# Kernel optimization log

Measured on AMD Instinct MI355X. Metric: run time of the kernel, lower is better.

The kernel has to match this reference:

```python
import jax, jax.numpy as jnp
import numpy as np

N = 100000      # nodes
DEG = 16        # in-degree per node
E = N * DEG     # edges
IN_DIM = 128
OUT_DIM = 32
EPS = 1e-8      # torch cosine_similarity norm clamp


def setup_inputs() -> dict:
    key = jax.random.key(0)
    k1, k2, k3, k4 = jax.random.split(key, 4)
    h = jax.random.normal(k1, (N, IN_DIM), dtype=jnp.float32)
    # xavier_uniform-scaled linear weight, shape [out_dim, in_dim] like nn.Linear
    W = jax.random.normal(k2, (OUT_DIM, IN_DIM), dtype=jnp.float32) * (1.0 / np.sqrt(IN_DIM))
    beta = jax.random.uniform(k3, (1,), dtype=jnp.float32)
    src = jax.random.randint(k4, (E,), 0, N)
    dst = jnp.arange(E) // DEG  # each node gets exactly DEG incoming edges
    return {"h": h, "W": W, "beta": beta, "src": src, "dst": dst}


def reference(h, W, beta, src, dst):
    # Note: F.dropout(p=0.6) from the original is omitted for a deterministic reference.
    z = h @ W.T                                   # [N, out_dim]
    zs = z[src]                                   # [E, out_dim] gather src features
    zd = z[dst]                                   # [E, out_dim] gather dst features
    num = jnp.sum(zs * zd, axis=-1)               # [E]
    ns = jnp.maximum(jnp.linalg.norm(zs, axis=-1), EPS)
    nd = jnp.maximum(jnp.linalg.norm(zd, axis=-1), EPS)
    cos = num / (ns * nd)                         # torch.cosine_similarity
    e = -beta[0] * (1.0 - cos)                    # [E] edge score
    # segment softmax over incoming edges of each dst node (stable)
    m = jax.ops.segment_max(e, dst, num_segments=N)
    m = jnp.where(jnp.isfinite(m), m, 0.0)        # guard isolated nodes
    ex = jnp.exp(e - m[dst])                      # [E]
    denom = jax.ops.segment_sum(ex, dst, num_segments=N)
    alpha = ex / denom[dst]                       # [E] attention weights
    # weighted scatter-sum of src features to dst nodes
    return jax.ops.segment_sum(alpha[:, None] * zs, dst, num_segments=N)  # [N, out_dim]
```

## Files before the change

### kernel.cpp

```cpp
#include <hip/hip_runtime.h>

#define IN_DIM 128
#define OUT_DIM 32
#define DEG 16
#define EPS 1e-8f
#define TN 64
#define HSTR 129

#define SWZ(x, p) __int_as_float(__builtin_amdgcn_ds_swizzle(__float_as_int(x), (p)))

__global__ __launch_bounds__(256) void gemm_norm_kernel(
    const float* __restrict__ h, const float* __restrict__ W,
    float* __restrict__ z, float* __restrict__ inv_nrm, int N) {
  __shared__ float sh[TN * HSTR];
  __shared__ float ssq[4][TN];

  const int tid = threadIdx.x;
  const int nb = blockIdx.x * TN;

  const float4* __restrict__ hg = (const float4*)h;
#pragma unroll
  for (int i = 0; i < 8; ++i) {
    const int f = tid + 256 * i;
    const int nd = f >> 5;
    const int k4 = f & 31;
    int gn = nb + nd;
    if (gn >= N) gn = N - 1;
    const float4 v = hg[(size_t)gn * 32 + k4];
    float* d = &sh[nd * HSTR + k4 * 4];
    d[0] = v.x; d[1] = v.y; d[2] = v.z; d[3] = v.w;
  }
  __syncthreads();

  const int w = __builtin_amdgcn_readfirstlane(tid >> 6);
  const int l = tid & 63;
  const int node = nb + l;
  const float* __restrict__ wb = W + (size_t)(w * 8) * IN_DIM;
  const float* hrow = &sh[l * HSTR];

  float acc[8] = {0.f, 0.f, 0.f, 0.f, 0.f, 0.f, 0.f, 0.f};
#pragma unroll 8
  for (int k = 0; k < IN_DIM; ++k) {
    const float hv = hrow[k];
#pragma unroll
    for (int j = 0; j < 8; ++j)
      acc[j] = fmaf(hv, wb[j * IN_DIM + k], acc[j]);
  }

  float ssp = 0.f;
#pragma unroll
  for (int j = 0; j < 8; ++j) ssp = fmaf(acc[j], acc[j], ssp);
  ssq[w][l] = ssp;

  if (node < N) {
    float4* zp = (float4*)(z + (size_t)node * OUT_DIM + w * 8);
    zp[0] = make_float4(acc[0], acc[1], acc[2], acc[3]);
    zp[1] = make_float4(acc[4], acc[5], acc[6], acc[7]);
  }
  __syncthreads();
  if (w == 0) {
    const float s = ssq[0][l] + ssq[1][l] + ssq[2][l] + ssq[3][l];
    if (node < N) inv_nrm[node] = 1.0f / fmaxf(sqrtf(s), EPS);
  }
}

__global__ __launch_bounds__(256) void edge_kernel(
    const float* __restrict__ z, const float* __restrict__ inv_nrm,
    const int* __restrict__ src, const float* __restrict__ beta_p,
    float* __restrict__ out, int N) {
  __shared__ float xp[4 * 2 * DEG * 36];

  const int tid = threadIdx.x;
  const int l = tid & 63, l5 = l & 31, half = l >> 5, wv = tid >> 6;
  const int gw = blockIdx.x * 4 + wv;
  if (gw * 2 >= N) return;
  const int n = gw * 2 + half;
  const int ne = (n < N) ? n : N - 1;
  const int e = l5 >> 1, c = l5 & 1;

  const float beta = *beta_p;
  const int se = src[(size_t)ne * DEG + e];
  const float inv_s = inv_nrm[se];
  const float inv_d = inv_nrm[ne];

  const float4* zs4 = (const float4*)(z + (size_t)se * OUT_DIM + c * 16);
  const float4 v0 = zs4[0], v1 = zs4[1], v2 = zs4[2], v3 = zs4[3];
  const float4* zd4 = (const float4*)(z + (size_t)ne * OUT_DIM + c * 16);
  const float4 d0 = zd4[0], d1 = zd4[1], d2 = zd4[2], d3 = zd4[3];

  float p = v0.x * d0.x;
  p = fmaf(v0.y, d0.y, p); p = fmaf(v0.z, d0.z, p); p = fmaf(v0.w, d0.w, p);
  p = fmaf(v1.x, d1.x, p); p = fmaf(v1.y, d1.y, p); p = fmaf(v1.z, d1.z, p);
  p = fmaf(v1.w, d1.w, p);
  p = fmaf(v2.x, d2.x, p); p = fmaf(v2.y, d2.y, p); p = fmaf(v2.z, d2.z, p);
  p = fmaf(v2.w, d2.w, p);
  p = fmaf(v3.x, d3.x, p); p = fmaf(v3.y, d3.y, p); p = fmaf(v3.z, d3.z, p);
  p = fmaf(v3.w, d3.w, p);
  p += SWZ(p, 0x041F);

  const float cosv = p * inv_s * inv_d;
  const float ex = __expf(beta * (cosv - 1.0f));

  float den = ex;
  den += SWZ(den, 0x081F);
  den += SWZ(den, 0x101F);
  den += SWZ(den, 0x201F);
  den += SWZ(den, 0x401F);
  const float rd = 1.0f / den;

  float* slot = xp + (wv * 2 + half) * (DEG * 36);
  float4* wp = (float4*)(slot + e * 36 + c * 16);
  wp[0] = make_float4(ex * v0.x, ex * v0.y, ex * v0.z, ex * v0.w);
  wp[1] = make_float4(ex * v1.x, ex * v1.y, ex * v1.z, ex * v1.w);
  wp[2] = make_float4(ex * v2.x, ex * v2.y, ex * v2.z, ex * v2.w);
  wp[3] = make_float4(ex * v3.x, ex * v3.y, ex * v3.z, ex * v3.w);

  float s = 0.f;
#pragma unroll
  for (int e2 = 0; e2 < DEG; ++e2)
    s += slot[e2 * 36 + l5];

  if (n < N) out[(size_t)n * OUT_DIM + l5] = s * rd;
}

extern "C" void kernel_launch(void* const* d_in, const int* in_sizes, int n_in,
                              void* d_out, int out_size, void* d_ws, size_t ws_size,
                              hipStream_t stream) {
  const float* h    = (const float*)d_in[0];
  const float* W    = (const float*)d_in[1];
  const float* beta = (const float*)d_in[2];
  const int*   src  = (const int*)d_in[3];

  const int N = in_sizes[0] / IN_DIM;

  float* z    = (float*)d_ws;
  float* invn = z + (size_t)N * OUT_DIM;

  const int bl1 = (N + TN - 1) / TN;
  gemm_norm_kernel<<<bl1, 256, 0, stream>>>(h, W, z, invn, N);

  const int waves2 = (N + 1) / 2;
  const int bl2 = (waves2 + 3) / 4;
  edge_kernel<<<bl2, 256, 0, stream>>>(z, invn, src, beta, (float*)d_out, N);
}
```

Measured before the change: 139.1 us.

## Store pre-normalized z as bf16 and transpose h tile for float4 LDS reads

```diff
diff --git a/kernel.cpp b/kernel.cpp
--- a/kernel.cpp
+++ b/kernel.cpp
@@ -5,73 +5,87 @@
 #define DEG 16
 #define EPS 1e-8f
 #define TN 64
-#define HSTR 129
+#define S4 65
 
 #define SWZ(x, p) __int_as_float(__builtin_amdgcn_ds_swizzle(__float_as_int(x), (p)))
 
+static __device__ __forceinline__ unsigned f2bf(float x) {
+  unsigned u = __float_as_uint(x);
+  u += 0x7FFFu + ((u >> 16) & 1u);
+  return u >> 16;
+}
+static __device__ __forceinline__ float bflo(unsigned u) { return __uint_as_float(u << 16); }
+static __device__ __forceinline__ float bfhi(unsigned u) { return __uint_as_float(u & 0xFFFF0000u); }
+
 __global__ __launch_bounds__(256) void gemm_norm_kernel(
     const float* __restrict__ h, const float* __restrict__ W,
-    float* __restrict__ z, float* __restrict__ inv_nrm, int N) {
-  __shared__ float sh[TN * HSTR];
+    unsigned short* __restrict__ zhb, float* __restrict__ nrm, int N) {
+  __shared__ float4 sh4[32 * S4];
   __shared__ float ssq[4][TN];
 
   const int tid = threadIdx.x;
   const int nb = blockIdx.x * TN;
 
-  const float4* __restrict__ hg = (const float4*)h;
+  {
+    const int k4 = tid & 31, r0 = tid >> 5;
+    const float4* __restrict__ hg = (const float4*)h;
 #pragma unroll
-  for (int i = 0; i < 8; ++i) {
-    const int f = tid + 256 * i;
-    const int nd = f >> 5;
-    const int k4 = f & 31;
-    int gn = nb + nd;
-    if (gn >= N) gn = N - 1;
-    const float4 v = hg[(size_t)gn * 32 + k4];
-    float* d = &sh[nd * HSTR + k4 * 4];
-    d[0] = v.x; d[1] = v.y; d[2] = v.z; d[3] = v.w;
+    for (int i = 0; i < 8; ++i) {
+      const int n = r0 + i * 8;
+      int gn = nb + n;
+      if (gn >= N) gn = N - 1;
+      sh4[k4 * S4 + n] = hg[(size_t)gn * 32 + k4];
+    }
   }
   __syncthreads();
 
-  const int w = __builtin_amdgcn_readfirstlane(tid >> 6);
+  const int w = tid >> 6;
   const int l = tid & 63;
   const int node = nb + l;
   const float* __restrict__ wb = W + (size_t)(w * 8) * IN_DIM;
-  const float* hrow = &sh[l * HSTR];
 
   float acc[8] = {0.f, 0.f, 0.f, 0.f, 0.f, 0.f, 0.f, 0.f};
-#pragma unroll 8
-  for (int k = 0; k < IN_DIM; ++k) {
-    const float hv = hrow[k];
+#pragma unroll 4
+  for (int k4 = 0; k4 < 32; ++k4) {
+    const float4 hv = sh4[k4 * S4 + l];
 #pragma unroll
-    for (int j = 0; j < 8; ++j)
-      acc[j] = fmaf(hv, wb[j * IN_DIM + k], acc[j]);
+    for (int j = 0; j < 8; ++j) {
+      const float* __restrict__ wr = wb + j * IN_DIM + k4 * 4;
+      acc[j] = fmaf(hv.x, wr[0], acc[j]);
+      acc[j] = fmaf(hv.y, wr[1], acc[j]);
+      acc[j] = fmaf(hv.z, wr[2], acc[j]);
+      acc[j] = fmaf(hv.w, wr[3], acc[j]);
+    }
   }
 
   float ssp = 0.f;
 #pragma unroll
   for (int j = 0; j < 8; ++j) ssp = fmaf(acc[j], acc[j], ssp);
   ssq[w][l] = ssp;
+  __syncthreads();
+  const float ss = ssq[0][l] + ssq[1][l] + ssq[2][l] + ssq[3][l];
+  const float ns = sqrtf(ss);
+  const float inv = 1.0f / fmaxf(ns, EPS);
 
   if (node < N) {
-    float4* zp = (float4*)(z + (size_t)node * OUT_DIM + w * 8);
-    zp[0] = make_float4(acc[0], acc[1], acc[2], acc[3]);
-    zp[1] = make_float4(acc[4], acc[5], acc[6], acc[7]);
-  }
-  __syncthreads();
-  if (w == 0) {
-    const float s = ssq[0][l] + ssq[1][l] + ssq[2][l] + ssq[3][l];
-    if (node < N) inv_nrm[node] = 1.0f / fmaxf(sqrtf(s), EPS);
+    unsigned p0 = f2bf(acc[0] * inv) | (f2bf(acc[1] * inv) << 16);
+    unsigned p1 = f2bf(acc[2] * inv) | (f2bf(acc[3] * inv) << 16);
+    unsigned p2 = f2bf(acc[4] * inv) | (f2bf(acc[5] * inv) << 16);
+    unsigned p3 = f2bf(acc[6] * inv) | (f2bf(acc[7] * inv) << 16);
+    uint4* zp = (uint4*)(zhb + (size_t)node * OUT_DIM + w * 8);
+    *zp = make_uint4(p0, p1, p2, p3);
+    if (w == 0) nrm[node] = ns;
   }
 }
 
 __global__ __launch_bounds__(256) void edge_kernel(
-    const float* __restrict__ z, const float* __restrict__ inv_nrm,
+    const unsigned short* __restrict__ zhb, const float* __restrict__ nrm,
     const int* __restrict__ src, const float* __restrict__ beta_p,
     float* __restrict__ out, int N) {
-  __shared__ float xp[4 * 2 * DEG * 36];
+  __shared__ float xp[8 * DEG * 36];
 
   const int tid = threadIdx.x;
-  const int l = tid & 63, l5 = l & 31, half = l >> 5, wv = tid >> 6;
+  const int l5 = tid & 31, half = (tid >> 5) & 1, wv = tid >> 6;
   const int gw = blockIdx.x * 4 + wv;
   if (gw * 2 >= N) return;
   const int n = gw * 2 + half;
@@ -80,26 +94,30 @@
 
   const float beta = *beta_p;
   const int se = src[(size_t)ne * DEG + e];
-  const float inv_s = inv_nrm[se];
-  const float inv_d = inv_nrm[ne];
+  const float nrm_s = nrm[se];
 
-  const float4* zs4 = (const float4*)(z + (size_t)se * OUT_DIM + c * 16);
-  const float4 v0 = zs4[0], v1 = zs4[1], v2 = zs4[2], v3 = zs4[3];
-  const float4* zd4 = (const float4*)(z + (size_t)ne * OUT_DIM + c * 16);
-  const float4 d0 = zd4[0], d1 = zd4[1], d2 = zd4[2], d3 = zd4[3];
+  const uint4* zs4 = (const uint4*)(zhb + (size_t)se * OUT_DIM) + c * 2;
+  const uint4 sa = zs4[0], sb = zs4[1];
+  const uint4* zd4 = (const uint4*)(zhb + (size_t)ne * OUT_DIM) + c * 2;
+  const uint4 da = zd4[0], db = zd4[1];
 
-  float p = v0.x * d0.x;
-  p = fmaf(v0.y, d0.y, p); p = fmaf(v0.z, d0.z, p); p = fmaf(v0.w, d0.w, p);
-  p = fmaf(v1.x, d1.x, p); p = fmaf(v1.y, d1.y, p); p = fmaf(v1.z, d1.z, p);
-  p = fmaf(v1.w, d1.w, p);
-  p = fmaf(v2.x, d2.x, p); p = fmaf(v2.y, d2.y, p); p = fmaf(v2.z, d2.z, p);
-  p = fmaf(v2.w, d2.w, p);
-  p = fmaf(v3.x, d3.x, p); p = fmaf(v3.y, d3.y, p); p = fmaf(v3.z, d3.z, p);
-  p = fmaf(v3.w, d3.w, p);
+  float vs[16];
+  vs[0] = bflo(sa.x);  vs[1] = bfhi(sa.x);  vs[2] = bflo(sa.y);  vs[3] = bfhi(sa.y);
+  vs[4] = bflo(sa.z);  vs[5] = bfhi(sa.z);  vs[6] = bflo(sa.w);  vs[7] = bfhi(sa.w);
+  vs[8] = bflo(sb.x);  vs[9] = bfhi(sb.x);  vs[10] = bflo(sb.y); vs[11] = bfhi(sb.y);
+  vs[12] = bflo(sb.z); vs[13] = bfhi(sb.z); vs[14] = bflo(sb.w); vs[15] = bfhi(sb.w);
+  float vd[16];
+  vd[0] = bflo(da.x);  vd[1] = bfhi(da.x);  vd[2] = bflo(da.y);  vd[3] = bfhi(da.y);
+  vd[4] = bflo(da.z);  vd[5] = bfhi(da.z);  vd[6] = bflo(da.w);  vd[7] = bfhi(da.w);
+  vd[8] = bflo(db.x);  vd[9] = bfhi(db.x);  vd[10] = bflo(db.y); vd[11] = bfhi(db.y);
+  vd[12] = bflo(db.z); vd[13] = bfhi(db.z); vd[14] = bflo(db.w); vd[15] = bfhi(db.w);
+
+  float p = vs[0] * vd[0];
+#pragma unroll
+  for (int i = 1; i < 16; ++i) p = fmaf(vs[i], vd[i], p);
   p += SWZ(p, 0x041F);
 
-  const float cosv = p * inv_s * inv_d;
-  const float ex = __expf(beta * (cosv - 1.0f));
+  const float ex = __expf(beta * (p - 1.0f));
 
   float den = ex;
   den += SWZ(den, 0x081F);
@@ -108,12 +126,13 @@
   den += SWZ(den, 0x401F);
   const float rd = 1.0f / den;
 
+  const float sc = ex * nrm_s;
   float* slot = xp + (wv * 2 + half) * (DEG * 36);
   float4* wp = (float4*)(slot + e * 36 + c * 16);
-  wp[0] = make_float4(ex * v0.x, ex * v0.y, ex * v0.z, ex * v0.w);
-  wp[1] = make_float4(ex * v1.x, ex * v1.y, ex * v1.z, ex * v1.w);
-  wp[2] = make_float4(ex * v2.x, ex * v2.y, ex * v2.z, ex * v2.w);
-  wp[3] = make_float4(ex * v3.x, ex * v3.y, ex * v3.z, ex * v3.w);
+  wp[0] = make_float4(sc * vs[0], sc * vs[1], sc * vs[2], sc * vs[3]);
+  wp[1] = make_float4(sc * vs[4], sc * vs[5], sc * vs[6], sc * vs[7]);
+  wp[2] = make_float4(sc * vs[8], sc * vs[9], sc * vs[10], sc * vs[11]);
+  wp[3] = make_float4(sc * vs[12], sc * vs[13], sc * vs[14], sc * vs[15]);
 
   float s = 0.f;
 #pragma unroll
@@ -133,13 +152,12 @@
 
   const int N = in_sizes[0] / IN_DIM;
 
-  float* z    = (float*)d_ws;
-  float* invn = z + (size_t)N * OUT_DIM;
+  unsigned short* zhb = (unsigned short*)d_ws;
+  float* nrm = (float*)(zhb + (size_t)N * OUT_DIM);
 
   const int bl1 = (N + TN - 1) / TN;
-  gemm_norm_kernel<<<bl1, 256, 0, stream>>>(h, W, z, invn, N);
+  gemm_norm_kernel<<<bl1, 256, 0, stream>>>(h, W, zhb, nrm, N);
 
-  const int waves2 = (N + 1) / 2;
-  const int bl2 = (waves2 + 3) / 4;
-  edge_kernel<<<bl2, 256, 0, stream>>>(z, invn, src, beta, (float*)d_out, N);
+  const int bl2 = ((N + 1) / 2 + 3) / 4;
+  edge_kernel<<<bl2, 256, 0, stream>>>(zhb, nrm, src, beta, (float*)d_out, N);
 }
```

After: 166.0 us. 1.19x slower.
